# Kernel tuning notes

Measured on AMD Instinct MI355X. Metric: run time of the kernel, lower is better.

## Reference

```python
import jax, jax.numpy as jnp
import numpy as np


def setup_inputs() -> dict:
    key = jax.random.key(0)
    kq, kk, kv = jax.random.split(key, 3)
    B, L, S, H, E, D = 2, 2048, 2048, 16, 64, 64
    return {
        "queries": jax.random.normal(kq, (B, L, H, E), dtype=jnp.float32),
        "keys": jax.random.normal(kk, (B, S, H, E), dtype=jnp.float32),
        "values": jax.random.normal(kv, (B, S, H, D), dtype=jnp.float32),
    }


def reference(queries, keys, values):
    # FullAttention forward (mask_flag=False, dropout=0.0 -> identity)
    E = queries.shape[-1]
    scale = 1.0 / jnp.sqrt(jnp.asarray(E, dtype=queries.dtype))
    # scores: [B, H, L, S]
    scores = jnp.einsum('blhe,bshe->bhls', queries, keys)
    A = jax.nn.softmax(scale * scores, axis=-1)
    # output: [B, L, H, D]
    V = jnp.einsum('bhls,bshd->blhd', A, values)
    return V
```

## Files before the change

### kernel.cpp

```cpp
#include <hip/hip_runtime.h>
#include <hip/hip_bf16.h>
#include <string.h>


#define NB 2
#define LL 2048
#define SS 2048
#define HH 16
#define EE 64
#define DD 64
#define KVB 64
#define NT (SS / KVB)
#define NWG2 (NB * HH * (LL / 64))

typedef _Float16 f16x8 __attribute__((ext_vector_type(8)));
typedef float f32x4 __attribute__((ext_vector_type(4)));
typedef float f32x16 __attribute__((ext_vector_type(16)));
typedef unsigned uint2v __attribute__((ext_vector_type(2)));
typedef unsigned uint4v __attribute__((ext_vector_type(4)));
typedef const __attribute__((address_space(1))) void* gas_p;
typedef __attribute__((address_space(3))) void* las_p;

__device__ __forceinline__ unsigned pk2h(float a, float b) {
    auto h = __builtin_amdgcn_cvt_pkrtz(a, b);
    unsigned u;
    __builtin_memcpy(&u, &h, 4);
    return u;
}

__device__ __forceinline__ float fexp2(float x) {
#if defined(__has_builtin) && __has_builtin(__builtin_amdgcn_exp2f)
    return __builtin_amdgcn_exp2f(x);
#else
    return exp2f(x);
#endif
}

__device__ __forceinline__ void gll16(const void* g, void* l) {
    __builtin_amdgcn_global_load_lds((gas_p)g, (las_p)l, 16, 0, 0);
}

__device__ __forceinline__ uint2v plswap(unsigned a, unsigned b) {
#if defined(__has_builtin) && __has_builtin(__builtin_amdgcn_permlane32_swap)
    return __builtin_amdgcn_permlane32_swap(a, b, false, false);
#else
    unsigned ax = (unsigned)__shfl_xor((int)a, 32);
    unsigned bx = (unsigned)__shfl_xor((int)b, 32);
    int l32 = (int)(threadIdx.x & 32);
    uint2v r;
    r[0] = l32 ? bx : a;
    r[1] = l32 ? b : ax;
    return r;
#endif
}

__device__ __forceinline__ float fbits(unsigned u) {
    float f; __builtin_memcpy(&f, &u, 4); return f;
}
__device__ __forceinline__ unsigned ubits(float f) {
    unsigned u; __builtin_memcpy(&u, &f, 4); return u;
}
__device__ __forceinline__ float xmax32(float x) {
    uint2v r = plswap(ubits(x), ubits(x));
    return fmaxf(fbits(r[0]), fbits(r[1]));
}
__device__ __forceinline__ float xsum32(float x) {
    uint2v r = plswap(ubits(x), ubits(x));
    return fbits(r[0]) + fbits(r[1]);
}

__global__ __launch_bounds__(256) void prepKV(const float* __restrict__ K,
                                              const float* __restrict__ V,
                                              unsigned short* __restrict__ Kh,
                                              unsigned short* __restrict__ Vth) {
    const int NTILE = NB * HH * NT;
    const bool isV = blockIdx.x >= NTILE;
    const int tile = blockIdx.x & (NTILE - 1);
    const int it = tile & (NT - 1);
    const int bh = tile >> 5;
    const int b = bh >> 4, h = bh & 15;
    const int t = threadIdx.x;

    if (!isV) {
        const int s = t >> 2, ec = t & 3;
        const float* src = K + (((size_t)b * SS + it * KVB + s) * HH + h) * EE + ec * 16;
        f32x4 x0 = ((const f32x4*)src)[0];
        f32x4 x1 = ((const f32x4*)src)[1];
        f32x4 x2 = ((const f32x4*)src)[2];
        f32x4 x3 = ((const f32x4*)src)[3];
        uint4v c0, c1;
        c0.x = pk2h(x0[0], x0[1]); c0.y = pk2h(x0[2], x0[3]);
        c0.z = pk2h(x1[0], x1[1]); c0.w = pk2h(x1[2], x1[3]);
        c1.x = pk2h(x2[0], x2[1]); c1.y = pk2h(x2[2], x2[3]);
        c1.z = pk2h(x3[0], x3[1]); c1.w = pk2h(x3[2], x3[3]);
        char* dst = (char*)Kh + (size_t)tile * 8192;
        const int sw = (s & 7) << 4;
        *(uint4v*)(dst + ((s * 128 + ec * 32) ^ sw)) = c0;
        *(uint4v*)(dst + ((s * 128 + ec * 32 + 16) ^ sw)) = c1;
    } else {
        __shared__ float Vt[64 * 68];
        {
            const int s = t >> 2, dc = t & 3;
            const float* src = V + (((size_t)b * SS + it * KVB + s) * HH + h) * DD + dc * 16;
            f32x4 x0 = ((const f32x4*)src)[0];
            f32x4 x1 = ((const f32x4*)src)[1];
            f32x4 x2 = ((const f32x4*)src)[2];
            f32x4 x3 = ((const f32x4*)src)[3];
            float* row = Vt + s * 68 + dc * 16;
            ((f32x4*)row)[0] = x0; ((f32x4*)row)[1] = x1;
            ((f32x4*)row)[2] = x2; ((f32x4*)row)[3] = x3;
        }
        __syncthreads();
        {
            const int d = t >> 2, sc = t & 3;
            float w[16];
#pragma unroll
            for (int j = 0; j < 16; ++j) w[j] = Vt[(sc * 16 + j) * 68 + d];
            uint4v c0, c1;
            c0.x = pk2h(w[0], w[1]); c0.y = pk2h(w[2], w[3]);
            c0.z = pk2h(w[4], w[5]); c0.w = pk2h(w[6], w[7]);
            c1.x = pk2h(w[8], w[9]); c1.y = pk2h(w[10], w[11]);
            c1.z = pk2h(w[12], w[13]); c1.w = pk2h(w[14], w[15]);
            char* dst = (char*)Vth + (size_t)tile * 8192;
            const int sw = (d & 7) << 4;
            *(uint4v*)(dst + ((d * 128 + sc * 32) ^ sw)) = c0;
            *(uint4v*)(dst + ((d * 128 + sc * 32 + 16) ^ sw)) = c1;
        }
    }
}

__global__ __launch_bounds__(256, 4) void fattn6(const unsigned short* __restrict__ Kh,
                                                 const unsigned short* __restrict__ Vth,
                                                 const float* __restrict__ Q,
                                                 float* __restrict__ O) {
    __shared__ __align__(16) char LB[18432];
    char* KA = LB;
    char* KB = LB + 8192;

    const int tid = threadIdx.x;
    const int lane = tid & 63;
    const int wid = tid >> 6;
    const int ln = lane & 31;
    const int hi = lane >> 5;
    const int qg = wid >> 1;
    const int sh = wid & 1;

    const int bid0 = blockIdx.x;
    const int bid = (bid0 & 7) * (NWG2 >> 3) + (bid0 >> 3);
    const int bh = bid >> 5;
    const int qt = bid & 31;
    const int b = bh >> 4, h = bh & 15;
    const int qrow = qt * 64 + qg * 32 + ln;

    const float qs = 0.125f * 1.44269504088896340736f;
    const float* qptr = Q + (((size_t)b * LL + qrow) * HH + h) * EE + hi * 8;
    f16x8 qf[4];
#pragma unroll
    for (int ks = 0; ks < 4; ++ks) {
        f32x4 a0 = *(const f32x4*)(qptr + ks * 16);
        f32x4 a1 = *(const f32x4*)(qptr + ks * 16 + 4);
        union { f16x8 v; unsigned u[4]; } cv;
        cv.u[0] = pk2h(a0[0] * qs, a0[1] * qs);
        cv.u[1] = pk2h(a0[2] * qs, a0[3] * qs);
        cv.u[2] = pk2h(a1[0] * qs, a1[1] * qs);
        cv.u[3] = pk2h(a1[2] * qs, a1[3] * qs);
        qf[ks] = cv.v;
    }

    f32x16 o0, o1;
#pragma unroll
    for (int i = 0; i < 16; ++i) { o0[i] = 0.f; o1[i] = 0.f; }
    float m = 0.f, l = 0.f;

    const char* Kg = (const char*)Kh + (size_t)bh * (NT * 8192);
    const char* vt = (const char*)Vth + (size_t)bh * (NT * 8192);

    const int swz = (ln & 7) << 4;
    const int srow = sh * 32 + ln;
    const int vcol = sh * 64;
    const int vo00 = (ln * 128 + vcol + hi * 16) ^ swz;
    const int vo01 = ((32 + ln) * 128 + vcol + hi * 16) ^ swz;
    const int vo10 = (ln * 128 + vcol + 32 + hi * 16) ^ swz;
    const int vo11 = ((32 + ln) * 128 + vcol + 32 + hi * 16) ^ swz;

    auto STAGE_K = [&](int it, char* Ks) {
        const size_t off = (size_t)it * 8192 + wid * 2048 + lane * 16;
        gll16(Kg + off, Ks + wid * 2048);
        gll16(Kg + off + 1024, Ks + wid * 2048 + 1024);
    };

    auto BODY = [&](const char* Ks) {
        f16x8 v00 = *(const f16x8*)(vt + vo00);
        f16x8 v01 = *(const f16x8*)(vt + vo01);
        f16x8 v10 = *(const f16x8*)(vt + vo10);
        f16x8 v11 = *(const f16x8*)(vt + vo11);
        vt += 8192;

        f32x16 st;
#pragma unroll
        for (int i = 0; i < 16; ++i) st[i] = -m;
        __builtin_amdgcn_s_setprio(1);
#pragma unroll
        for (int ks = 0; ks < 4; ++ks) {
            f16x8 kf = *(const f16x8*)(Ks + ((srow * 128 + ks * 32 + hi * 16) ^ swz));
            st = __builtin_amdgcn_mfma_f32_32x32x16_f16(kf, qf[ks], st, 0, 0, 0);
        }
        __builtin_amdgcn_s_setprio(0);

        float x0 = fmaxf(fmaxf(st[0], st[4]), fmaxf(st[8], st[12]));
        float x1 = fmaxf(fmaxf(st[1], st[5]), fmaxf(st[9], st[13]));
        float x2 = fmaxf(fmaxf(st[2], st[6]), fmaxf(st[10], st[14]));
        float x3 = fmaxf(fmaxf(st[3], st[7]), fmaxf(st[11], st[15]));
        float pmax = xmax32(fmaxf(fmaxf(x0, x1), fmaxf(x2, x3)));
        if (!__all(pmax <= 8.0f)) {
            const float delta = fminf(0.f, -pmax);
            const float al = fexp2(delta);
            l *= al;
            m += fmaxf(0.f, pmax);
#pragma unroll
            for (int i = 0; i < 16; ++i) { o0[i] *= al; o1[i] *= al; }
#pragma unroll
            for (int i = 0; i < 16; ++i) st[i] += delta;
        }
        float t0 = 0.f, t1 = 0.f, t2 = 0.f, t3 = 0.f;
#pragma unroll
        for (int r = 0; r < 16; r += 4) {
            st[r] = fexp2(st[r]);
            st[r + 1] = fexp2(st[r + 1]);
            st[r + 2] = fexp2(st[r + 2]);
            st[r + 3] = fexp2(st[r + 3]);
            t0 += st[r]; t1 += st[r + 1]; t2 += st[r + 2]; t3 += st[r + 3];
        }
        l += (t0 + t1) + (t2 + t3);

        {
            uint2v r0 = plswap(pk2h(st[0], st[1]), pk2h(st[4], st[5]));
            uint2v r1 = plswap(pk2h(st[2], st[3]), pk2h(st[6], st[7]));
            union { f16x8 v; unsigned u[4]; } w;
            w.u[0] = r0[0]; w.u[1] = r1[0]; w.u[2] = r0[1]; w.u[3] = r1[1];
            __builtin_amdgcn_s_setprio(1);
            o0 = __builtin_amdgcn_mfma_f32_32x32x16_f16(v00, w.v, o0, 0, 0, 0);
            o1 = __builtin_amdgcn_mfma_f32_32x32x16_f16(v01, w.v, o1, 0, 0, 0);
            __builtin_amdgcn_s_setprio(0);
        }
        {
            uint2v r2 = plswap(pk2h(st[8], st[9]), pk2h(st[12], st[13]));
            uint2v r3 = plswap(pk2h(st[10], st[11]), pk2h(st[14], st[15]));
            union { f16x8 v; unsigned u[4]; } w;
            w.u[0] = r2[0]; w.u[1] = r3[0]; w.u[2] = r2[1]; w.u[3] = r3[1];
            __builtin_amdgcn_s_setprio(1);
            o0 = __builtin_amdgcn_mfma_f32_32x32x16_f16(v10, w.v, o0, 0, 0, 0);
            o1 = __builtin_amdgcn_mfma_f32_32x32x16_f16(v11, w.v, o1, 0, 0, 0);
            __builtin_amdgcn_s_setprio(0);
        }
    };

    STAGE_K(0, KA);
    __syncthreads();
    for (int t = 0; t < NT; t += 2) {
        if (t + 1 < NT) STAGE_K(t + 1, KB);
        BODY(KA);
        __syncthreads();
        if (t + 2 < NT) STAGE_K(t + 2, KA);
        BODY(KB);
        __syncthreads();
    }

    float* msh = (float*)(LB + 16896);
    float* lsh = (float*)(LB + 17408);
    l = xsum32(l);
    if (hi == 0) { msh[wid * 32 + ln] = m; lsh[wid * 32 + ln] = l; }
    __syncthreads();
    const float mo = msh[(wid ^ 1) * 32 + ln];
    const float lo = lsh[(wid ^ 1) * 32 + ln];
    const float ms = fmaxf(m, mo);
    const float f = fexp2(m - ms);
    const float fo = fexp2(mo - ms);
    const float lstar = l * f + lo * fo;

    float* pbuf = (float*)LB + qg * (32 * 65);
    if (sh == 1) {
#pragma unroll
        for (int r = 0; r < 16; ++r) {
            const int d = (r & 3) + 8 * (r >> 2) + 4 * hi;
            pbuf[ln * 65 + d] = o0[r] * f;
            pbuf[ln * 65 + 32 + d] = o1[r] * f;
        }
    }
    __syncthreads();
    if (sh == 0) {
        const float invl = 1.f / lstar;
        float* optr = O + (((size_t)b * LL + qrow) * HH + h) * DD;
#pragma unroll
        for (int t = 0; t < 4; ++t) {
            f32x4 w0, w1;
#pragma unroll
            for (int i = 0; i < 4; ++i) {
                const int d = t * 8 + hi * 4 + i;
                w0[i] = (o0[4 * t + i] * f + pbuf[ln * 65 + d]) * invl;
                w1[i] = (o1[4 * t + i] * f + pbuf[ln * 65 + 32 + d]) * invl;
            }
            *(f32x4*)(optr + t * 8 + hi * 4) = w0;
            *(f32x4*)(optr + 32 + t * 8 + hi * 4) = w1;
        }
    }
}

typedef unsigned u2f __attribute__((ext_vector_type(2)));
__global__ __launch_bounds__(256) void fattn1(const float* __restrict__ Q,
                                              const float* __restrict__ K,
                                              const float* __restrict__ V,
                                              float* __restrict__ O) {
    __shared__ __align__(16) short Klds[KVB * 64];
    __shared__ __align__(16) short Vtlds[64 * KVB];
    __shared__ __align__(16) short Plds[4][16 * 64];

    const int tid = threadIdx.x;
    const int lane = tid & 63;
    const int wid = tid >> 6;
    const int g = (lane >> 4) & 3;
    const int c = lane & 15;

    const int bid = blockIdx.x;
    const int bh = bid >> 5;
    const int qt = bid & 31;
    const int b = bh >> 4;
    const int h = bh & 15;
    const int q0 = qt * 64;

    const int qrow = q0 + wid * 16 + c;
    const float* qptr = Q + (((size_t)b * LL + qrow) * HH + h) * EE;
    const float qs = 0.125f * 1.44269504088896340736f;
    f16x8 qf[2];
#pragma unroll
    for (int kk = 0; kk < 2; ++kk) {
        f32x4 a0 = *(const f32x4*)(qptr + kk * 32 + g * 8);
        f32x4 a1 = *(const f32x4*)(qptr + kk * 32 + g * 8 + 4);
        union { f16x8 v; unsigned u[4]; } cv;
        cv.u[0] = pk2h(a0[0] * qs, a0[1] * qs);
        cv.u[1] = pk2h(a0[2] * qs, a0[3] * qs);
        cv.u[2] = pk2h(a1[0] * qs, a1[1] * qs);
        cv.u[3] = pk2h(a1[2] * qs, a1[3] * qs);
        qf[kk] = cv.v;
    }

    f32x4 osacc[4];
    const f32x4 fzero = {0.f, 0.f, 0.f, 0.f};
#pragma unroll
    for (int i = 0; i < 4; ++i) osacc[i] = fzero;
    float m_run = -1e30f;
    float l_run = 0.f;

    const int km = tid & 15;
    const int kr = tid >> 4;

    for (int it = 0; it < NT; ++it) {
        const int s_glob = it * KVB;
        f32x4 kreg[4];
#pragma unroll
        for (int p = 0; p < 4; ++p) {
            int s = kr + p * 16;
            kreg[p] = *(const f32x4*)(K + (((size_t)b * SS + s_glob + s) * HH + h) * EE + km * 4);
        }
        f32x4 vreg[4];
#pragma unroll
        for (int p = 0; p < 4; ++p) {
            int s = kr * 4 + p;
            vreg[p] = *(const f32x4*)(V + (((size_t)b * SS + s_glob + s) * HH + h) * DD + km * 4);
        }
        __syncthreads();
#pragma unroll
        for (int p = 0; p < 4; ++p) {
            int s = kr + p * 16;
            u2f w;
            w.x = pk2h(kreg[p][0], kreg[p][1]);
            w.y = pk2h(kreg[p][2], kreg[p][3]);
            int byte = (s * 128 + km * 8) ^ ((s & 7) << 4);
            *(u2f*)((char*)Klds + byte) = w;
        }
#pragma unroll
        for (int i = 0; i < 4; ++i) {
            int d = km * 4 + i;
            u2f w;
            w.x = pk2h(vreg[0][i], vreg[1][i]);
            w.y = pk2h(vreg[2][i], vreg[3][i]);
            int byte = (d * 128 + kr * 8) ^ ((d & 7) << 4);
            *(u2f*)((char*)Vtlds + byte) = w;
        }
        __syncthreads();

        f32x4 stv[4];
#pragma unroll
        for (int fr = 0; fr < 4; ++fr) stv[fr] = fzero;
#pragma unroll
        for (int fr = 0; fr < 4; ++fr) {
            int s = fr * 16 + c;
            f16x8 kf0 = *(const f16x8*)((const char*)Klds + ((s * 128 + 16 * g) ^ ((s & 7) << 4)));
            stv[fr] = __builtin_amdgcn_mfma_f32_16x16x32_f16(kf0, qf[0], stv[fr], 0, 0, 0);
            f16x8 kf1 = *(const f16x8*)((const char*)Klds + ((s * 128 + 64 + 16 * g) ^ ((s & 7) << 4)));
            stv[fr] = __builtin_amdgcn_mfma_f32_16x16x32_f16(kf1, qf[1], stv[fr], 0, 0, 0);
        }

        float pmax = stv[0][0];
#pragma unroll
        for (int fr = 0; fr < 4; ++fr)
#pragma unroll
            for (int r = 0; r < 4; ++r) pmax = fmaxf(pmax, stv[fr][r]);
        pmax = fmaxf(pmax, __shfl_xor(pmax, 16));
        pmax = fmaxf(pmax, __shfl_xor(pmax, 32));
        float mnew = fmaxf(m_run, pmax);
        float alpha = fexp2(m_run - mnew);
        float tsum = 0.f;
#pragma unroll
        for (int fr = 0; fr < 4; ++fr)
#pragma unroll
            for (int r = 0; r < 4; ++r) {
                float e = fexp2(stv[fr][r] - mnew);
                stv[fr][r] = e;
                tsum += e;
            }
        tsum += __shfl_xor(tsum, 16);
        tsum += __shfl_xor(tsum, 32);
        l_run = l_run * alpha + tsum;
        m_run = mnew;
#pragma unroll
        for (int fr = 0; fr < 4; ++fr)
#pragma unroll
            for (int r = 0; r < 4; ++r) osacc[fr][r] *= alpha;

        short* plb = &Plds[wid][0];
#pragma unroll
        for (int fr = 0; fr < 4; ++fr) {
            u2f w;
            w.x = pk2h(stv[fr][0], stv[fr][1]);
            w.y = pk2h(stv[fr][2], stv[fr][3]);
            int byte = (c * 128 + fr * 32 + g * 8) ^ ((c & 7) << 4);
            *(u2f*)((char*)plb + byte) = w;
        }
        f16x8 pb0 = *(const f16x8*)((const char*)plb + ((c * 128 + 16 * g) ^ ((c & 7) << 4)));
        f16x8 pb1 = *(const f16x8*)((const char*)plb + ((c * 128 + 64 + 16 * g) ^ ((c & 7) << 4)));

#pragma unroll
        for (int fr = 0; fr < 4; ++fr) {
            int d = fr * 16 + c;
            f16x8 vf0 = *(const f16x8*)((const char*)Vtlds + ((d * 128 + 16 * g) ^ ((d & 7) << 4)));
            osacc[fr] = __builtin_amdgcn_mfma_f32_16x16x32_f16(vf0, pb0, osacc[fr], 0, 0, 0);
            f16x8 vf1 = *(const f16x8*)((const char*)Vtlds + ((d * 128 + 64 + 16 * g) ^ ((d & 7) << 4)));
            osacc[fr] = __builtin_amdgcn_mfma_f32_16x16x32_f16(vf1, pb1, osacc[fr], 0, 0, 0);
        }
    }

    float invl = 1.f / l_run;
    float* optr = O + (((size_t)b * LL + qrow) * HH + h) * DD;
#pragma unroll
    for (int fr = 0; fr < 4; ++fr) {
        f32x4 o;
        o[0] = osacc[fr][0] * invl;
        o[1] = osacc[fr][1] * invl;
        o[2] = osacc[fr][2] * invl;
        o[3] = osacc[fr][3] * invl;
        *(f32x4*)(optr + fr * 16 + g * 4) = o;
    }
}

extern "C" void kernel_launch(void* const* d_in, const int* in_sizes, int n_in,
                              void* d_out, int out_size, void* d_ws, size_t ws_size,
                              hipStream_t stream) {
    const float* Q = (const float*)d_in[0];
    const float* K = (const float*)d_in[1];
    const float* V = (const float*)d_in[2];
    float* Op = (float*)d_out;

    const size_t halfBytes = (size_t)NB * HH * SS * EE * 2;
    if (ws_size >= 2 * halfBytes) {
        unsigned short* Kht = (unsigned short*)d_ws;
        unsigned short* Vht = (unsigned short*)((char*)d_ws + halfBytes);
        hipLaunchKernelGGL(prepKV, dim3(2 * NB * HH * NT), dim3(256), 0, stream, K, V, Kht, Vht);
        hipLaunchKernelGGL(fattn6, dim3(NWG2), dim3(256), 0, stream, Kht, Vht, Q, Op);
    } else {
        hipLaunchKernelGGL(fattn1, dim3(NB * HH * (LL / 64)), dim3(256), 0, stream, Q, K, V, Op);
    }
}
```

Measured before the change: 68.73 us.

## Load K fragments directly from global memory instead of staging through LDS

```diff
diff --git a/kernel.cpp b/kernel.cpp
--- a/kernel.cpp
+++ b/kernel.cpp
@@ -18,8 +18,6 @@
 typedef float f32x16 __attribute__((ext_vector_type(16)));
 typedef unsigned uint2v __attribute__((ext_vector_type(2)));
 typedef unsigned uint4v __attribute__((ext_vector_type(4)));
-typedef const __attribute__((address_space(1))) void* gas_p;
-typedef __attribute__((address_space(3))) void* las_p;
 
 __device__ __forceinline__ unsigned pk2h(float a, float b) {
     auto h = __builtin_amdgcn_cvt_pkrtz(a, b);
@@ -34,10 +32,6 @@
 #else
     return exp2f(x);
 #endif
-}
-
-__device__ __forceinline__ void gll16(const void* g, void* l) {
-    __builtin_amdgcn_global_load_lds((gas_p)g, (las_p)l, 16, 0, 0);
 }
 
 __device__ __forceinline__ uint2v plswap(unsigned a, unsigned b) {
@@ -129,13 +123,11 @@
     }
 }
 
-__global__ __launch_bounds__(256, 4) void fattn6(const unsigned short* __restrict__ Kh,
+__global__ __launch_bounds__(256, 4) void fattn7(const unsigned short* __restrict__ Kh,
                                                  const unsigned short* __restrict__ Vth,
                                                  const float* __restrict__ Q,
                                                  float* __restrict__ O) {
     __shared__ __align__(16) char LB[18432];
-    char* KA = LB;
-    char* KB = LB + 8192;
 
     const int tid = threadIdx.x;
     const int lane = tid & 63;
@@ -172,39 +164,41 @@
     for (int i = 0; i < 16; ++i) { o0[i] = 0.f; o1[i] = 0.f; }
     float m = 0.f, l = 0.f;
 
-    const char* Kg = (const char*)Kh + (size_t)bh * (NT * 8192);
+    const char* kt = (const char*)Kh + (size_t)bh * (NT * 8192);
     const char* vt = (const char*)Vth + (size_t)bh * (NT * 8192);
 
     const int swz = (ln & 7) << 4;
     const int srow = sh * 32 + ln;
     const int vcol = sh * 64;
+    const int ko0 = (srow * 128 + 0 * 32 + hi * 16) ^ swz;
+    const int ko1 = (srow * 128 + 1 * 32 + hi * 16) ^ swz;
+    const int ko2 = (srow * 128 + 2 * 32 + hi * 16) ^ swz;
+    const int ko3 = (srow * 128 + 3 * 32 + hi * 16) ^ swz;
     const int vo00 = (ln * 128 + vcol + hi * 16) ^ swz;
     const int vo01 = ((32 + ln) * 128 + vcol + hi * 16) ^ swz;
     const int vo10 = (ln * 128 + vcol + 32 + hi * 16) ^ swz;
     const int vo11 = ((32 + ln) * 128 + vcol + 32 + hi * 16) ^ swz;
 
-    auto STAGE_K = [&](int it, char* Ks) {
-        const size_t off = (size_t)it * 8192 + wid * 2048 + lane * 16;
-        gll16(Kg + off, Ks + wid * 2048);
-        gll16(Kg + off + 1024, Ks + wid * 2048 + 1024);
-    };
-
-    auto BODY = [&](const char* Ks) {
+    for (int t = 0; t < NT; ++t) {
+        f16x8 k0 = *(const f16x8*)(kt + ko0);
+        f16x8 k1 = *(const f16x8*)(kt + ko1);
+        f16x8 k2 = *(const f16x8*)(kt + ko2);
+        f16x8 k3 = *(const f16x8*)(kt + ko3);
         f16x8 v00 = *(const f16x8*)(vt + vo00);
         f16x8 v01 = *(const f16x8*)(vt + vo01);
         f16x8 v10 = *(const f16x8*)(vt + vo10);
         f16x8 v11 = *(const f16x8*)(vt + vo11);
+        kt += 8192;
         vt += 8192;
 
         f32x16 st;
 #pragma unroll
         for (int i = 0; i < 16; ++i) st[i] = -m;
         __builtin_amdgcn_s_setprio(1);
-#pragma unroll
-        for (int ks = 0; ks < 4; ++ks) {
-            f16x8 kf = *(const f16x8*)(Ks + ((srow * 128 + ks * 32 + hi * 16) ^ swz));
-            st = __builtin_amdgcn_mfma_f32_32x32x16_f16(kf, qf[ks], st, 0, 0, 0);
-        }
+        st = __builtin_amdgcn_mfma_f32_32x32x16_f16(k0, qf[0], st, 0, 0, 0);
+        st = __builtin_amdgcn_mfma_f32_32x32x16_f16(k1, qf[1], st, 0, 0, 0);
+        st = __builtin_amdgcn_mfma_f32_32x32x16_f16(k2, qf[2], st, 0, 0, 0);
+        st = __builtin_amdgcn_mfma_f32_32x32x16_f16(k3, qf[3], st, 0, 0, 0);
         __builtin_amdgcn_s_setprio(0);
 
         float x0 = fmaxf(fmaxf(st[0], st[4]), fmaxf(st[8], st[12]));
@@ -253,17 +247,6 @@
             o1 = __builtin_amdgcn_mfma_f32_32x32x16_f16(v11, w.v, o1, 0, 0, 0);
             __builtin_amdgcn_s_setprio(0);
         }
-    };
-
-    STAGE_K(0, KA);
-    __syncthreads();
-    for (int t = 0; t < NT; t += 2) {
-        if (t + 1 < NT) STAGE_K(t + 1, KB);
-        BODY(KA);
-        __syncthreads();
-        if (t + 2 < NT) STAGE_K(t + 2, KA);
-        BODY(KB);
-        __syncthreads();
     }
 
     float* msh = (float*)(LB + 16896);
@@ -476,7 +459,7 @@
         unsigned short* Kht = (unsigned short*)d_ws;
         unsigned short* Vht = (unsigned short*)((char*)d_ws + halfBytes);
         hipLaunchKernelGGL(prepKV, dim3(2 * NB * HH * NT), dim3(256), 0, stream, K, V, Kht, Vht);
-        hipLaunchKernelGGL(fattn6, dim3(NWG2), dim3(256), 0, stream, Kht, Vht, Q, Op);
+        hipLaunchKernelGGL(fattn7, dim3(NWG2), dim3(256), 0, stream, Kht, Vht, Q, Op);
     } else {
         hipLaunchKernelGGL(fattn1, dim3(NB * HH * (LL / 64)), dim3(256), 0, stream, Q, K, V, Op);
     }
```

New measurement: 75.19 us. 9.4% more time.
